# Kernel optimization log

Hardware: AMD Instinct MI355X
Metric: run time of the kernel (lower is better)

The kernel has to match this reference:

```python
import jax, jax.numpy as jnp
import numpy as np

# Algorithm constants (scaled-down but structure-identical to the source:
# original Nxy=2304, Nz=300, ItN=60, ROISize=300, NxyExt=128, BkgMean=110, SNR=200)
ItN = 2
BkgMean = 110.0
ROISize = 256
SNR = 200.0
NxyExt = 64
Nxy = 1024
Nz = 24
LO = Nxy // 2 - ROISize   # ROI start inside the padded FFT plane
HI = Nxy // 2 + ROISize   # ROI end


def setup_inputs() -> dict:
    key = jax.random.key(0)
    k1, k2, k3, k4 = jax.random.split(key, 4)
    # raw camera image; uniform in [0, 400) so that subtracting BkgMean=110 keeps signal
    imstack = jax.random.uniform(k1, (1, 1, Nxy - 2 * NxyExt, Nxy - 2 * NxyExt), dtype=jnp.float32) * 400.0
    # initial object volume estimate (the `init` ctor arg)
    init_vol = jax.random.uniform(k2, (1, Nz, 2 * ROISize, 2 * ROISize), dtype=jnp.float32)
    # learned frequency-domain PSF kernel (rand * 0.001, as in __init__)
    conv_real = jax.random.uniform(k3, (1, 1, Nxy, Nxy), dtype=jnp.float32) * 0.001
    conv_imag = jax.random.uniform(k4, (1, 1, Nxy, Nxy), dtype=jnp.float32) * 0.001
    return {"imstack": imstack, "init_vol": init_vol, "conv_real": conv_real, "conv_imag": conv_imag}


def reference(imstack, init_vol, conv_real, conv_imag):
    # Complex frequency-domain kernel; constant across iterations (the source
    # rebuilds/casts it every slice -- same math, hoisted here).
    K = (conv_real + 1j * conv_imag)[0, 0]            # [Nxy, Nxy] complex
    Ksum = jnp.sum(conv_real)

    img = jnp.maximum(imstack - BkgMean, 0.0)
    ImgExp = jnp.pad(img, ((0, 0), (0, 0), (NxyExt, NxyExt), (NxyExt, NxyExt)))  # [1,1,Nxy,Nxy]

    obj = init_vol                                     # [1, Nz, 2R, 2R]
    for _ in range(ItN):
        # --- forward projection: batched over all Nz slices (source loops) ---
        # each slice is placed into the center ROI of a zero [Nxy,Nxy] plane
        vol = jnp.pad(obj, ((0, 0), (0, 0), (LO, Nxy - HI), (LO, Nxy - HI)))  # [1,Nz,Nxy,Nxy]
        est = jnp.real(jnp.fft.ifft2(jnp.fft.fft2(vol) * K)) / Ksum
        ImgEst = jnp.sum(jnp.maximum(est, 0.0), axis=1, keepdims=True)        # [1,1,Nxy,Nxy]

        # --- ratio image (interior only; border stays 1) ---
        Tmp = jnp.median(ImgEst)
        inner = ImgExp[:, :, NxyExt:-NxyExt, NxyExt:-NxyExt] / (
            ImgEst[:, :, NxyExt:-NxyExt, NxyExt:-NxyExt] + Tmp / SNR)
        Ratio = jnp.ones((1, 1, Nxy, Nxy), dtype=ImgEst.dtype)
        Ratio = Ratio.at[:, :, NxyExt:-NxyExt, NxyExt:-NxyExt].set(inner)

        # --- back projection: in the source, fft2(Ratio)*conj(K) is identical for
        # every jj (Ratio and K do not change inside the loop), so compute once ---
        back = jnp.real(jnp.fft.ifft2(jnp.fft.fft2(Ratio) * jnp.conj(K))) / Ksum
        back = jnp.maximum(back, 0.0)                  # [1,1,Nxy,Nxy]
        obj = obj * back[:, :, LO:HI, LO:HI]           # broadcast over Nz
    return obj
```

## Files before the change

kernel.cpp:

```cpp
#include <hip/hip_runtime.h>
#include <math.h>

#define NXY  1024
#define NZ   24
#define ROI2 512
#define LO_  256
#define EXT  64
#define IMGW 896
#define ITN  2
#define SNR_ 200.0f
#define BKG  110.0f
#define RANK1 524287u
#define RANK2 524288u
#define NACC 8
#define PAD(i) ((i) + ((i) >> 4))

typedef float2 cf;

__device__ __forceinline__ cf cadd(cf a, cf b) { return make_float2(a.x + b.x, a.y + b.y); }
__device__ __forceinline__ cf csub(cf a, cf b) { return make_float2(a.x - b.x, a.y - b.y); }
__device__ __forceinline__ cf cmul(cf a, cf b) { return make_float2(a.x * b.x - a.y * b.y, a.x * b.y + a.y * b.x); }

__device__ __forceinline__ void twinit(cf* TW) {
  int k = threadIdx.x;
  float s, c;
  sincosf(-6.28318530717958647692f * (float)k / 1024.0f, &s, &c);
  TW[k] = make_float2(c, s);
}

template <int SIGN>
__device__ cf* fft1024_r4(cf* src, cf* dst, const cf* TW) {
  const int tid = threadIdx.x;
#pragma unroll
  for (int t = 0; t < 5; ++t) {
    __syncthreads();
    const int s = 1 << (2 * t);
    const int q = tid & (s - 1);
    const int sp = tid - q;
    cf a0 = src[PAD(tid)];
    cf a1 = src[PAD(tid + 256)];
    cf a2 = src[PAD(tid + 512)];
    cf a3 = src[PAD(tid + 768)];
    cf b0 = cadd(a0, a2), b1 = csub(a0, a2);
    cf b2 = cadd(a1, a3), b3 = csub(a1, a3);
    cf jb3 = (SIGN < 0) ? make_float2(b3.y, -b3.x) : make_float2(-b3.y, b3.x);
    cf c0 = cadd(b0, b2);
    cf c2 = csub(b0, b2);
    cf c1 = cadd(b1, jb3);
    cf c3 = csub(b1, jb3);
    cf t1v = TW[sp];
    if (SIGN > 0) t1v.y = -t1v.y;
    cf t2v = cmul(t1v, t1v);
    cf t3v = cmul(t2v, t1v);
    const int base = 4 * tid - 3 * q;
    dst[PAD(base)]         = c0;
    dst[PAD(base + s)]     = cmul(c1, t1v);
    dst[PAD(base + 2 * s)] = cmul(c2, t2v);
    dst[PAD(base + 3 * s)] = cmul(c3, t3v);
    cf* tmp = src; src = dst; dst = tmp;
  }
  __syncthreads();
  return src;
}

__global__ void ksum_kernel(const float* __restrict__ a, float* __restrict__ out) {
  __shared__ float s[256];
  int tid = threadIdx.x;
  float acc = 0.f;
  for (int i = blockIdx.x * 256 + tid; i < NXY * NXY; i += gridDim.x * 256) acc += a[i];
  s[tid] = acc;
  __syncthreads();
  for (int o = 128; o > 0; o >>= 1) {
    if (tid < o) s[tid] += s[tid + o];
    __syncthreads();
  }
  if (tid == 0) atomicAdd(out, s[0]);
}

__global__ void imgexp_kernel(const float* __restrict__ im, float* __restrict__ out) {
  int idx = blockIdx.x * 256 + threadIdx.x;
  int r = idx >> 10, c = idx & 1023;
  float v = 0.f;
  if (r >= EXT && r < NXY - EXT && c >= EXT && c < NXY - EXT) {
    float t = im[(size_t)(r - EXT) * IMGW + (c - EXT)] - BKG;
    v = t > 0.f ? t : 0.f;
  }
  out[idx] = v;
}

__global__ void buildkh_kernel(const float* __restrict__ kre, const float* __restrict__ kim,
                               cf* __restrict__ kt) {
  int idx = blockIdx.x * 256 + threadIdx.x;
  if (idx >= 513 * 1024) return;
  int ky = idx & 1023, kx = idx >> 10;
  int ny = (1024 - ky) & 1023, nx = (1024 - kx) & 1023;
  float ar = kre[(size_t)ky * NXY + kx], ai = kim[(size_t)ky * NXY + kx];
  float br = kre[(size_t)ny * NXY + nx], bi = kim[(size_t)ny * NXY + nx];
  kt[idx] = make_float2(0.5f * (ar + br), 0.5f * (ai - bi));
}

__global__ void transpose_kernel(const cf* __restrict__ in, cf* __restrict__ out, int R, int C) {
  __shared__ cf tile[32][33];
  size_t zoff = (size_t)blockIdx.z * R * C;
  const cf* src = in + zoff;
  cf* dst = out + zoff;
  int bc = blockIdx.x * 32, br = blockIdx.y * 32;
  int tx = threadIdx.x, ty = threadIdx.y;
#pragma unroll
  for (int j = 0; j < 32; j += 8) tile[ty + j][tx] = src[(size_t)(br + ty + j) * C + bc + tx];
  __syncthreads();
#pragma unroll
  for (int j = 0; j < 32; j += 8) dst[(size_t)(bc + ty + j) * R + br + tx] = tile[tx][ty + j];
}

__global__ __launch_bounds__(256) void pass1_kernel(const float* __restrict__ in, int rowLen, int rowOff,
                                                    cf* __restrict__ out) {
  __shared__ cf X[1088], Y[1088], TW[256];
  int tid = threadIdx.x;
  int b = blockIdx.x, zl = blockIdx.y;
  int nrows = 2 * gridDim.x;
  twinit(TW);
  const float* r0 = in + ((size_t)zl * nrows + 2 * b) * rowLen;
  const float* r1 = r0 + rowLen;
  for (int k = tid; k < 1024; k += 256) {
    cf v = make_float2(0.f, 0.f);
    if (k >= rowOff && k < rowOff + rowLen) { v.x = r0[k - rowOff]; v.y = r1[k - rowOff]; }
    X[PAD(k)] = v;
  }
  cf* G = fft1024_r4<-1>(X, Y, TW);
  cf* o0 = out + ((size_t)zl * nrows + 2 * b) * 512;
  cf* o1 = o0 + 512;
  for (int k = tid; k < 512; k += 256) {
    if (k == 0) {
      cf g0 = G[PAD(0)], gn = G[PAD(512)];
      o0[0] = make_float2(g0.x, gn.x);
      o1[0] = make_float2(g0.y, gn.y);
    } else {
      cf c = G[PAD(k)], d = G[PAD(1024 - k)];
      o0[k] = make_float2(0.5f * (c.x + d.x), 0.5f * (c.y - d.y));
      o1[k] = make_float2(0.5f * (c.y + d.y), 0.5f * (d.x - c.x));
    }
  }
}

__global__ __launch_bounds__(256) void pass1b_kernel(const float* __restrict__ iexp,
                                                     const float* __restrict__ iest,
                                                     const float* __restrict__ tos,
                                                     cf* __restrict__ out) {
  __shared__ cf X[1088], Y[1088], TW[256];
  int tid = threadIdx.x, b = blockIdx.x;
  twinit(TW);
  float t = tos[0];
  int r0 = 2 * b, r1 = 2 * b + 1;
  bool in0 = (r0 >= EXT && r0 < NXY - EXT);
  bool in1 = (r1 >= EXT && r1 < NXY - EXT);
  for (int k = tid; k < 1024; k += 256) {
    bool kin = (k >= EXT && k < NXY - EXT);
    float v0 = (in0 && kin) ? iexp[(size_t)r0 * NXY + k] / (iest[(size_t)r0 * NXY + k] + t) : 1.0f;
    float v1 = (in1 && kin) ? iexp[(size_t)r1 * NXY + k] / (iest[(size_t)r1 * NXY + k] + t) : 1.0f;
    X[PAD(k)] = make_float2(v0, v1);
  }
  cf* G = fft1024_r4<-1>(X, Y, TW);
  cf* o0 = out + (size_t)r0 * 512;
  cf* o1 = out + (size_t)r1 * 512;
  for (int k = tid; k < 512; k += 256) {
    if (k == 0) {
      cf g0 = G[PAD(0)], gn = G[PAD(512)];
      o0[0] = make_float2(g0.x, gn.x);
      o1[0] = make_float2(g0.y, gn.y);
    } else {
      cf c = G[PAD(k)], d = G[PAD(1024 - k)];
      o0[k] = make_float2(0.5f * (c.x + d.x), 0.5f * (c.y - d.y));
      o1[k] = make_float2(0.5f * (c.y + d.y), 0.5f * (d.x - c.x));
    }
  }
}

__global__ __launch_bounds__(256) void pass2_kernel(const cf* __restrict__ in, int inLen, int inOff,
                                                    const cf* __restrict__ kt, cf* __restrict__ out,
                                                    int zn, int ZB, int conjK) {
  __shared__ cf X[1088], Y[1088], TW[256];
  int tid = threadIdx.x;
  int kc = blockIdx.x;
  twinit(TW);
  const cf* krow = kt + (size_t)kc * NXY;
  cf kv[4];
#pragma unroll
  for (int j = 0; j < 4; ++j) {
    kv[j] = krow[tid + 256 * j];
    if (conjK) kv[j].y = -kv[j].y;
  }
  int srccol = (kc == 512) ? 0 : kc;
  int zlo = blockIdx.y * ZB, zhi = min(zn, zlo + ZB);
  for (int z = zlo; z < zhi; ++z) {
    const cf* src = in + ((size_t)z * 512 + srccol) * inLen;
    if (kc == 0 || kc == 512) {
      for (int k = tid; k < 1024; k += 256) {
        float v = 0.f;
        if (k >= inOff && k < inOff + inLen) {
          cf s = src[k - inOff];
          v = (kc == 0) ? s.x : s.y;
        }
        X[PAD(k)] = make_float2(v, 0.f);
      }
    } else {
      for (int k = tid; k < 1024; k += 256) {
        cf v = make_float2(0.f, 0.f);
        if (k >= inOff && k < inOff + inLen) v = src[k - inOff];
        X[PAD(k)] = v;
      }
    }
    cf* F = fft1024_r4<-1>(X, Y, TW);
#pragma unroll
    for (int j = 0; j < 4; ++j) {
      int p = PAD(tid + 256 * j);
      F[p] = cmul(F[p], kv[j]);
    }
    cf* G = fft1024_r4<1>(F, X, TW);
    cf* dstz = out + (size_t)z * 512 * NXY;
    if (kc == 0) {
      for (int k = tid; k < 1024; k += 256) dstz[k].x = G[PAD(k)].x;
    } else if (kc == 512) {
      for (int k = tid; k < 1024; k += 256) dstz[k].y = G[PAD(k)].x;
    } else {
      for (int k = tid; k < 1024; k += 256) dstz[(size_t)kc * NXY + k] = G[PAD(k)];
    }
    __syncthreads();
  }
}

__global__ __launch_bounds__(256) void pass3_fwd_kernel(const cf* __restrict__ in,
                                                        float* __restrict__ partials,
                                                        const float* __restrict__ ksump, int zn) {
  __shared__ cf X[1088], Y[1088], TW[256];
  int tid = threadIdx.x;
  int b = blockIdx.x, a = blockIdx.y;
  twinit(TW);
  float scale = 1.0f / (1048576.0f * ksump[0]);
  int r0 = 2 * b, r1 = 2 * b + 1;
  float acc[8] = {0.f, 0.f, 0.f, 0.f, 0.f, 0.f, 0.f, 0.f};
  for (int z = a; z < zn; z += NACC) {
    const cf* s0 = in + ((size_t)z * NXY + r0) * 512;
    const cf* s1 = s0 + 512;
    for (int k = tid; k < 512; k += 256) {
      cf u0 = s0[k], u1 = s1[k];
      if (k == 0) {
        X[PAD(0)]   = make_float2(u0.x, u1.x);
        X[PAD(512)] = make_float2(u0.y, u1.y);
      } else {
        X[PAD(k)]        = make_float2(u0.x - u1.y, u0.y + u1.x);
        X[PAD(1024 - k)] = make_float2(u0.x + u1.y, u1.x - u0.y);
      }
    }
    cf* G = fft1024_r4<1>(X, Y, TW);
#pragma unroll
    for (int j = 0; j < 4; ++j) {
      cf g = G[PAD(tid + 256 * j)];
      float v0 = g.x * scale, v1 = g.y * scale;
      acc[j]     += v0 > 0.f ? v0 : 0.f;
      acc[4 + j] += v1 > 0.f ? v1 : 0.f;
    }
    __syncthreads();
  }
  float* d0 = partials + ((size_t)a * NXY + r0) * NXY;
  float* d1 = d0 + NXY;
#pragma unroll
  for (int j = 0; j < 4; ++j) {
    d0[tid + 256 * j] += acc[j];
    d1[tid + 256 * j] += acc[4 + j];
  }
}

__global__ void fold_kernel(const float* __restrict__ partials, float* __restrict__ iest) {
  int i = blockIdx.x * 256 + threadIdx.x;
  float s = 0.f;
#pragma unroll
  for (int a = 0; a < NACC; ++a) s += partials[(size_t)a * NXY * NXY + i];
  iest[i] = s;
}

__global__ __launch_bounds__(256) void pass3_back_kernel(const cf* __restrict__ in, float* __restrict__ obj,
                                                         const float* __restrict__ ksump) {
  __shared__ cf X[1088], Y[1088], TW[256];
  __shared__ float br0[512], br1[512];
  int tid = threadIdx.x, b = blockIdx.x;
  twinit(TW);
  float scale = 1.0f / (1048576.0f * ksump[0]);
  int r0 = LO_ + 2 * b, r1 = r0 + 1;
  const cf* s0 = in + (size_t)r0 * 512;
  const cf* s1 = in + (size_t)r1 * 512;
  for (int k = tid; k < 512; k += 256) {
    cf u0 = s0[k], u1 = s1[k];
    if (k == 0) {
      X[PAD(0)]   = make_float2(u0.x, u1.x);
      X[PAD(512)] = make_float2(u0.y, u1.y);
    } else {
      X[PAD(k)]        = make_float2(u0.x - u1.y, u0.y + u1.x);
      X[PAD(1024 - k)] = make_float2(u0.x + u1.y, u1.x - u0.y);
    }
  }
  cf* G = fft1024_r4<1>(X, Y, TW);
  for (int k = tid; k < 512; k += 256) {
    cf g = G[PAD(k + LO_)];
    float v0 = g.x * scale, v1 = g.y * scale;
    br0[k] = v0 > 0.f ? v0 : 0.f;
    br1[k] = v1 > 0.f ? v1 : 0.f;
  }
  __syncthreads();
  int rp0 = 2 * b, rp1 = 2 * b + 1;
  for (int idx = tid; idx < NZ * 512; idx += 256) {
    int z = idx >> 9, c = idx & 511;
    obj[((size_t)z * ROI2 + rp0) * ROI2 + c] *= br0[c];
    obj[((size_t)z * ROI2 + rp1) * ROI2 + c] *= br1[c];
  }
}

__global__ void medinit_kernel(unsigned* st) {
  if (threadIdx.x == 0) { st[0] = 0u; st[1] = 0u; st[2] = RANK1; st[3] = RANK2; }
}

__global__ void medhist_kernel(const float* __restrict__ v, const unsigned* __restrict__ st,
                               unsigned* __restrict__ hist, int shift, unsigned maskHigh, int nb) {
  extern __shared__ unsigned h[];
  int tid = threadIdx.x;
  for (int k = tid; k < 2 * nb; k += 256) h[k] = 0u;
  __syncthreads();
  unsigned p1 = st[0], p2 = st[1];
  unsigned bm = (unsigned)(nb - 1);
  for (int i = blockIdx.x * 256 + tid; i < NXY * NXY; i += gridDim.x * 256) {
    unsigned u = __float_as_uint(v[i]);
    unsigned b = (u >> shift) & bm;
    if ((u & maskHigh) == (p1 & maskHigh)) atomicAdd(&h[b], 1u);
    if ((u & maskHigh) == (p2 & maskHigh)) atomicAdd(&h[nb + b], 1u);
  }
  __syncthreads();
  for (int k = tid; k < 2 * nb; k += 256) atomicAdd(&hist[k], h[k]);
}

__global__ void medpick_kernel(unsigned* st, const unsigned* __restrict__ hist, int shift, int nb,
                               int finalRound, float* tos) {
  __shared__ unsigned ps[256];
  int t = threadIdx.x;
  int per = nb >> 8;
  for (int which = 0; which < 2; ++which) {
    unsigned loc[8];
    unsigned my = 0;
    for (int i = 0; i < per; ++i) { loc[i] = hist[which * nb + t * per + i]; my += loc[i]; }
    ps[t] = my;
    __syncthreads();
    for (int off = 1; off < 256; off <<= 1) {
      unsigned v = (t >= off) ? ps[t - off] : 0u;
      __syncthreads();
      ps[t] += v;
      __syncthreads();
    }
    unsigned pre = ps[t] - my;
    unsigned r = st[2 + which];
    if (r >= pre && r < pre + my) {
      unsigned cum = pre;
      for (int i = 0; i < per; ++i) {
        if (r < cum + loc[i]) {
          st[which] |= (unsigned)(t * per + i) << shift;
          st[2 + which] = r - cum;
          break;
        }
        cum += loc[i];
      }
    }
    __syncthreads();
  }
  if (finalRound && t == 0) {
    float m = 0.5f * (__uint_as_float(st[0]) + __uint_as_float(st[1]));
    tos[0] = m / SNR_;
  }
}

extern "C" void kernel_launch(void* const* d_in, const int* in_sizes, int n_in,
                              void* d_out, int out_size, void* d_ws, size_t ws_size,
                              hipStream_t stream) {
  const float* imstack  = (const float*)d_in[0];
  const float* init_vol = (const float*)d_in[1];
  const float* conv_re  = (const float*)d_in[2];
  const float* conv_im  = (const float*)d_in[3];
  float* obj = (float*)d_out;

  char* w = (char*)d_ws;
  size_t off = 0;
  auto alloc = [&](size_t bytes) -> void* {
    void* p = (void*)(w + off);
    off += (bytes + 255) & ~(size_t)255;
    return p;
  };

  const size_t PLANE = (size_t)NXY * NXY;
  const size_t HPLANE = (size_t)512 * NXY;
  cf* KT         = (cf*)alloc((size_t)513 * NXY * sizeof(cf));
  float* IExp    = (float*)alloc(PLANE * 4);
  float* IEst    = (float*)alloc(PLANE * 4);
  float* Partial = (float*)alloc((size_t)NACC * PLANE * 4);
  float* Ksum    = (float*)alloc(256);
  unsigned* St   = (unsigned*)alloc(256);
  unsigned* Hist = (unsigned*)alloc(2 * 2048 * 4);
  size_t fixedEnd = off;

  int ZC = 1;
  const int zcs[8] = {24, 12, 8, 6, 4, 3, 2, 1};
  for (int i = 0; i < 8; ++i) {
    size_t need = fixedEnd + (size_t)zcs[i] * 2ull * HPLANE * sizeof(cf) + 4096;
    if (need <= ws_size) { ZC = zcs[i]; break; }
  }
  cf* bufC = (cf*)alloc((size_t)ZC * HPLANE * sizeof(cf));
  cf* bufD = (cf*)alloc((size_t)ZC * HPLANE * sizeof(cf));
  float* Tos = Ksum + 1;

  hipMemcpyAsync(obj, init_vol, (size_t)NZ * ROI2 * ROI2 * 4, hipMemcpyDeviceToDevice, stream);
  hipMemsetAsync(Ksum, 0, 8, stream);
  ksum_kernel<<<256, 256, 0, stream>>>(conv_re, Ksum);
  imgexp_kernel<<<4096, 256, 0, stream>>>(imstack, IExp);
  buildkh_kernel<<<2052, 256, 0, stream>>>(conv_re, conv_im, KT);

  const int shifts[3] = {21, 10, 0};
  const int nbs[3]    = {2048, 2048, 1024};
  const unsigned masks[3] = {0u, 0xFFE00000u, 0xFFFFFC00u};

  for (int it = 0; it < ITN; ++it) {
    hipMemsetAsync(Partial, 0, (size_t)NACC * PLANE * 4, stream);
    for (int z0 = 0; z0 < NZ; z0 += ZC) {
      int zn = (NZ - z0 < ZC) ? (NZ - z0) : ZC;
      int nzb = (zn + 3) / 4;
      pass1_kernel<<<dim3(256, zn), 256, 0, stream>>>(obj + (size_t)z0 * ROI2 * ROI2, ROI2, LO_, bufC);
      transpose_kernel<<<dim3(16, 16, zn), dim3(32, 8), 0, stream>>>(bufC, bufD, 512, 512);
      pass2_kernel<<<dim3(513, nzb), 256, 0, stream>>>(bufD, 512, LO_, KT, bufC, zn, 4, 0);
      transpose_kernel<<<dim3(32, 16, zn), dim3(32, 8), 0, stream>>>(bufC, bufD, 512, 1024);
      pass3_fwd_kernel<<<dim3(512, NACC), 256, 0, stream>>>(bufD, Partial, Ksum, zn);
    }
    fold_kernel<<<4096, 256, 0, stream>>>(Partial, IEst);
    medinit_kernel<<<1, 64, 0, stream>>>(St);
    for (int round = 0; round < 3; ++round) {
      hipMemsetAsync(Hist, 0, 2 * 2048 * 4, stream);
      medhist_kernel<<<256, 256, 2 * nbs[round] * 4, stream>>>(IEst, St, Hist, shifts[round],
                                                               masks[round], nbs[round]);
      medpick_kernel<<<1, 256, 0, stream>>>(St, Hist, shifts[round], nbs[round],
                                            round == 2 ? 1 : 0, Tos);
    }
    pass1b_kernel<<<512, 256, 0, stream>>>(IExp, IEst, Tos, bufC);
    transpose_kernel<<<dim3(16, 32, 1), dim3(32, 8), 0, stream>>>(bufC, bufD, 1024, 512);
    pass2_kernel<<<dim3(513, 1), 256, 0, stream>>>(bufD, 1024, 0, KT, bufC, 1, 1, 1);
    transpose_kernel<<<dim3(32, 16, 1), dim3(32, 8), 0, stream>>>(bufC, bufD, 512, 1024);
    pass3_back_kernel<<<256, 256, 0, stream>>>(bufD, obj, Ksum);
  }
}
```

Before: 705.9 us.

## Prune zero-input FFT stages, merge Nyquist columns, swizzle LDS, trim launches

```diff
diff --git a/kernel.cpp b/kernel.cpp
--- a/kernel.cpp
+++ b/kernel.cpp
@@ -12,8 +12,8 @@
 #define BKG  110.0f
 #define RANK1 524287u
 #define RANK2 524288u
-#define NACC 8
-#define PAD(i) ((i) + ((i) >> 4))
+#define NACC 4
+#define SWZ(i) ((i) ^ ((((i) >> 4) & 3) * 5))
 
 typedef float2 cf;
 
@@ -21,26 +21,31 @@
 __device__ __forceinline__ cf csub(cf a, cf b) { return make_float2(a.x - b.x, a.y - b.y); }
 __device__ __forceinline__ cf cmul(cf a, cf b) { return make_float2(a.x * b.x - a.y * b.y, a.x * b.y + a.y * b.x); }
 
-__device__ __forceinline__ void twinit(cf* TW) {
+struct Tw { const cf *t0, *t1, *t2, *t3; };
+
+__device__ __forceinline__ void twinit_all(cf* TW0, cf* T1, cf* T2, cf* T3) {
+  const float W = -6.28318530717958647692f / 1024.0f;
   int k = threadIdx.x;
   float s, c;
-  sincosf(-6.28318530717958647692f * (float)k / 1024.0f, &s, &c);
-  TW[k] = make_float2(c, s);
-}
-
-template <int SIGN>
-__device__ cf* fft1024_r4(cf* src, cf* dst, const cf* TW) {
+  sincosf(W * (float)k, &s, &c);
+  TW0[k] = make_float2(c, s);
+  if (k < 64) { sincosf(W * (float)(4 * k), &s, &c);  T1[k] = make_float2(c, s); }
+  if (k < 16) { sincosf(W * (float)(16 * k), &s, &c); T2[k] = make_float2(c, s); }
+  if (k < 4)  { sincosf(W * (float)(64 * k), &s, &c); T3[k] = make_float2(c, s); }
+}
+
+template <int SIGN, int T0>
+__device__ cf* fft1024_r4_t(cf* src, cf* dst, Tw tw) {
   const int tid = threadIdx.x;
 #pragma unroll
-  for (int t = 0; t < 5; ++t) {
+  for (int t = T0; t < 5; ++t) {
     __syncthreads();
     const int s = 1 << (2 * t);
     const int q = tid & (s - 1);
-    const int sp = tid - q;
-    cf a0 = src[PAD(tid)];
-    cf a1 = src[PAD(tid + 256)];
-    cf a2 = src[PAD(tid + 512)];
-    cf a3 = src[PAD(tid + 768)];
+    cf a0 = src[SWZ(tid)];
+    cf a1 = src[SWZ(tid + 256)];
+    cf a2 = src[SWZ(tid + 512)];
+    cf a3 = src[SWZ(tid + 768)];
     cf b0 = cadd(a0, a2), b1 = csub(a0, a2);
     cf b2 = cadd(a1, a3), b3 = csub(a1, a3);
     cf jb3 = (SIGN < 0) ? make_float2(b3.y, -b3.x) : make_float2(-b3.y, b3.x);
@@ -48,19 +53,45 @@
     cf c2 = csub(b0, b2);
     cf c1 = cadd(b1, jb3);
     cf c3 = csub(b1, jb3);
-    cf t1v = TW[sp];
-    if (SIGN > 0) t1v.y = -t1v.y;
-    cf t2v = cmul(t1v, t1v);
-    cf t3v = cmul(t2v, t1v);
     const int base = 4 * tid - 3 * q;
-    dst[PAD(base)]         = c0;
-    dst[PAD(base + s)]     = cmul(c1, t1v);
-    dst[PAD(base + 2 * s)] = cmul(c2, t2v);
-    dst[PAD(base + 3 * s)] = cmul(c3, t3v);
+    if (t == 4) {
+      dst[SWZ(base)]         = c0;
+      dst[SWZ(base + s)]     = c1;
+      dst[SWZ(base + 2 * s)] = c2;
+      dst[SWZ(base + 3 * s)] = c3;
+    } else {
+      cf t1v = (t == 0) ? tw.t0[tid] : (t == 1) ? tw.t1[tid >> 2]
+             : (t == 2) ? tw.t2[tid >> 4] : tw.t3[tid >> 6];
+      if (SIGN > 0) t1v.y = -t1v.y;
+      cf t2v = cmul(t1v, t1v);
+      cf t3v = cmul(t2v, t1v);
+      dst[SWZ(base)]         = c0;
+      dst[SWZ(base + s)]     = cmul(c1, t1v);
+      dst[SWZ(base + 2 * s)] = cmul(c2, t2v);
+      dst[SWZ(base + 3 * s)] = cmul(c3, t3v);
+    }
     cf* tmp = src; src = dst; dst = tmp;
   }
   __syncthreads();
   return src;
+}
+
+__device__ __forceinline__ void fft_stage0_half(cf a1, cf a2, cf* dst, const cf* TW0) {
+  const int tid = threadIdx.x;
+  cf b1 = make_float2(-a2.x, -a2.y);
+  cf jb3 = make_float2(a1.y, -a1.x);
+  cf c0 = cadd(a2, a1);
+  cf c2 = csub(a2, a1);
+  cf c1 = cadd(b1, jb3);
+  cf c3 = csub(b1, jb3);
+  cf t1v = TW0[tid];
+  cf t2v = cmul(t1v, t1v);
+  cf t3v = cmul(t2v, t1v);
+  const int base = 4 * tid;
+  dst[SWZ(base)]     = c0;
+  dst[SWZ(base + 1)] = cmul(c1, t1v);
+  dst[SWZ(base + 2)] = cmul(c2, t2v);
+  dst[SWZ(base + 3)] = cmul(c3, t3v);
 }
 
 __global__ void ksum_kernel(const float* __restrict__ a, float* __restrict__ out) {
@@ -113,30 +144,26 @@
   for (int j = 0; j < 32; j += 8) dst[(size_t)(bc + ty + j) * R + br + tx] = tile[tx][ty + j];
 }
 
-__global__ __launch_bounds__(256) void pass1_kernel(const float* __restrict__ in, int rowLen, int rowOff,
-                                                    cf* __restrict__ out) {
-  __shared__ cf X[1088], Y[1088], TW[256];
-  int tid = threadIdx.x;
-  int b = blockIdx.x, zl = blockIdx.y;
-  int nrows = 2 * gridDim.x;
-  twinit(TW);
-  const float* r0 = in + ((size_t)zl * nrows + 2 * b) * rowLen;
-  const float* r1 = r0 + rowLen;
-  for (int k = tid; k < 1024; k += 256) {
-    cf v = make_float2(0.f, 0.f);
-    if (k >= rowOff && k < rowOff + rowLen) { v.x = r0[k - rowOff]; v.y = r1[k - rowOff]; }
-    X[PAD(k)] = v;
-  }
-  cf* G = fft1024_r4<-1>(X, Y, TW);
-  cf* o0 = out + ((size_t)zl * nrows + 2 * b) * 512;
+__global__ __launch_bounds__(256) void pass1_kernel(const float* __restrict__ in, cf* __restrict__ out) {
+  __shared__ cf X[1024], Y[1024], TW0[256], T1[64], T2[16], T3[4];
+  int tid = threadIdx.x, b = blockIdx.x, zl = blockIdx.y;
+  twinit_all(TW0, T1, T2, T3);
+  const float* r0 = in + ((size_t)zl * 512 + 2 * b) * 512;
+  const float* r1 = r0 + 512;
+  cf a1 = make_float2(r0[tid], r1[tid]);
+  cf a2 = make_float2(r0[tid + 256], r1[tid + 256]);
+  fft_stage0_half(a1, a2, Y, TW0);
+  Tw tw{TW0, T1, T2, T3};
+  cf* G = fft1024_r4_t<-1, 1>(Y, X, tw);
+  cf* o0 = out + ((size_t)zl * 512 + 2 * b) * 512;
   cf* o1 = o0 + 512;
   for (int k = tid; k < 512; k += 256) {
     if (k == 0) {
-      cf g0 = G[PAD(0)], gn = G[PAD(512)];
+      cf g0 = G[SWZ(0)], gn = G[SWZ(512)];
       o0[0] = make_float2(g0.x, gn.x);
       o1[0] = make_float2(g0.y, gn.y);
     } else {
-      cf c = G[PAD(k)], d = G[PAD(1024 - k)];
+      cf c = G[SWZ(k)], d = G[SWZ(1024 - k)];
       o0[k] = make_float2(0.5f * (c.x + d.x), 0.5f * (c.y - d.y));
       o1[k] = make_float2(0.5f * (c.y + d.y), 0.5f * (d.x - c.x));
     }
@@ -147,9 +174,9 @@
                                                      const float* __restrict__ iest,
                                                      const float* __restrict__ tos,
                                                      cf* __restrict__ out) {
-  __shared__ cf X[1088], Y[1088], TW[256];
+  __shared__ cf X[1024], Y[1024], TW0[256], T1[64], T2[16], T3[4];
   int tid = threadIdx.x, b = blockIdx.x;
-  twinit(TW);
+  twinit_all(TW0, T1, T2, T3);
   float t = tos[0];
   int r0 = 2 * b, r1 = 2 * b + 1;
   bool in0 = (r0 >= EXT && r0 < NXY - EXT);
@@ -158,84 +185,98 @@
     bool kin = (k >= EXT && k < NXY - EXT);
     float v0 = (in0 && kin) ? iexp[(size_t)r0 * NXY + k] / (iest[(size_t)r0 * NXY + k] + t) : 1.0f;
     float v1 = (in1 && kin) ? iexp[(size_t)r1 * NXY + k] / (iest[(size_t)r1 * NXY + k] + t) : 1.0f;
-    X[PAD(k)] = make_float2(v0, v1);
-  }
-  cf* G = fft1024_r4<-1>(X, Y, TW);
+    X[SWZ(k)] = make_float2(v0, v1);
+  }
+  Tw tw{TW0, T1, T2, T3};
+  cf* G = fft1024_r4_t<-1, 0>(X, Y, tw);
   cf* o0 = out + (size_t)r0 * 512;
   cf* o1 = out + (size_t)r1 * 512;
   for (int k = tid; k < 512; k += 256) {
     if (k == 0) {
-      cf g0 = G[PAD(0)], gn = G[PAD(512)];
+      cf g0 = G[SWZ(0)], gn = G[SWZ(512)];
       o0[0] = make_float2(g0.x, gn.x);
       o1[0] = make_float2(g0.y, gn.y);
     } else {
-      cf c = G[PAD(k)], d = G[PAD(1024 - k)];
+      cf c = G[SWZ(k)], d = G[SWZ(1024 - k)];
       o0[k] = make_float2(0.5f * (c.x + d.x), 0.5f * (c.y - d.y));
       o1[k] = make_float2(0.5f * (c.y + d.y), 0.5f * (d.x - c.x));
     }
   }
 }
 
-__global__ __launch_bounds__(256) void pass2_kernel(const cf* __restrict__ in, int inLen, int inOff,
+template <int HALFIN>
+__global__ __launch_bounds__(256) void pass2_kernel(const cf* __restrict__ in,
                                                     const cf* __restrict__ kt, cf* __restrict__ out,
                                                     int zn, int ZB, int conjK) {
-  __shared__ cf X[1088], Y[1088], TW[256];
-  int tid = threadIdx.x;
-  int kc = blockIdx.x;
-  twinit(TW);
-  const cf* krow = kt + (size_t)kc * NXY;
-  cf kv[4];
+  __shared__ cf X[1024], Y[1024], TW0[256], T1[64], T2[16], T3[4];
+  int tid = threadIdx.x, kc = blockIdx.x;
+  twinit_all(TW0, T1, T2, T3);
+  Tw tw{TW0, T1, T2, T3};
+  cf kva[4], kvb[4];
 #pragma unroll
   for (int j = 0; j < 4; ++j) {
-    kv[j] = krow[tid + 256 * j];
-    if (conjK) kv[j].y = -kv[j].y;
-  }
-  int srccol = (kc == 512) ? 0 : kc;
+    kva[j] = kt[(size_t)kc * NXY + tid + 256 * j];
+    if (conjK) kva[j].y = -kva[j].y;
+  }
+  if (kc == 0) {
+#pragma unroll
+    for (int j = 0; j < 4; ++j) {
+      kvb[j] = kt[(size_t)512 * NXY + tid + 256 * j];
+      if (conjK) kvb[j].y = -kvb[j].y;
+    }
+  }
+  const int inLen = HALFIN ? 512 : 1024;
   int zlo = blockIdx.y * ZB, zhi = min(zn, zlo + ZB);
   for (int z = zlo; z < zhi; ++z) {
-    const cf* src = in + ((size_t)z * 512 + srccol) * inLen;
-    if (kc == 0 || kc == 512) {
-      for (int k = tid; k < 1024; k += 256) {
-        float v = 0.f;
-        if (k >= inOff && k < inOff + inLen) {
-          cf s = src[k - inOff];
-          v = (kc == 0) ? s.x : s.y;
-        }
-        X[PAD(k)] = make_float2(v, 0.f);
+    const cf* src = in + ((size_t)z * 512 + kc) * inLen;
+    cf* F;
+    if (HALFIN) {
+      cf a1 = src[tid], a2 = src[tid + 256];
+      fft_stage0_half(a1, a2, Y, TW0);
+      F = fft1024_r4_t<-1, 1>(Y, X, tw);
+    } else {
+      for (int k = tid; k < 1024; k += 256) X[SWZ(k)] = src[k];
+      F = fft1024_r4_t<-1, 0>(X, Y, tw);
+    }
+    if (kc == 0) {
+      cf fk[4], fn[4];
+#pragma unroll
+      for (int j = 0; j < 4; ++j) {
+        int k = tid + 256 * j, nk = (1024 - k) & 1023;
+        fk[j] = F[SWZ(k)];
+        fn[j] = F[SWZ(nk)];
       }
-    } else {
-      for (int k = tid; k < 1024; k += 256) {
-        cf v = make_float2(0.f, 0.f);
-        if (k >= inOff && k < inOff + inLen) v = src[k - inOff];
-        X[PAD(k)] = v;
+      __syncthreads();
+#pragma unroll
+      for (int j = 0; j < 4; ++j) {
+        int k = tid + 256 * j;
+        cf Fa = make_float2(0.5f * (fk[j].x + fn[j].x), 0.5f * (fk[j].y - fn[j].y));
+        cf Fb = make_float2(0.5f * (fk[j].y + fn[j].y), 0.5f * (fn[j].x - fk[j].x));
+        cf Ga = cmul(Fa, kva[j]);
+        cf Gb = cmul(Fb, kvb[j]);
+        F[SWZ(k)] = make_float2(Ga.x - Gb.y, Ga.y + Gb.x);
       }
-    }
-    cf* F = fft1024_r4<-1>(X, Y, TW);
-#pragma unroll
-    for (int j = 0; j < 4; ++j) {
-      int p = PAD(tid + 256 * j);
-      F[p] = cmul(F[p], kv[j]);
-    }
-    cf* G = fft1024_r4<1>(F, X, TW);
-    cf* dstz = out + (size_t)z * 512 * NXY;
-    if (kc == 0) {
-      for (int k = tid; k < 1024; k += 256) dstz[k].x = G[PAD(k)].x;
-    } else if (kc == 512) {
-      for (int k = tid; k < 1024; k += 256) dstz[k].y = G[PAD(k)].x;
-    } else {
-      for (int k = tid; k < 1024; k += 256) dstz[(size_t)kc * NXY + k] = G[PAD(k)];
-    }
-    __syncthreads();
+    } else {
+#pragma unroll
+      for (int j = 0; j < 4; ++j) {
+        int p = SWZ(tid + 256 * j);
+        F[p] = cmul(F[p], kva[j]);
+      }
+    }
+    cf* G = fft1024_r4_t<1, 0>(F, (F == X) ? Y : X, tw);
+    cf* dst = out + ((size_t)z * 512 + kc) * NXY;
+    for (int k = tid; k < 1024; k += 256) dst[k] = G[SWZ(k)];
   }
 }
 
 __global__ __launch_bounds__(256) void pass3_fwd_kernel(const cf* __restrict__ in,
                                                         float* __restrict__ partials,
-                                                        const float* __restrict__ ksump, int zn) {
-  __shared__ cf X[1088], Y[1088], TW[256];
-  int tid = threadIdx.x;
-  int b = blockIdx.x, a = blockIdx.y;
-  twinit(TW);
+                                                        const float* __restrict__ ksump, int zn,
+                                                        int accum) {
+  __shared__ cf X[1024], Y[1024], TW0[256], T1[64], T2[16], T3[4];
+  int tid = threadIdx.x, b = blockIdx.x, a = blockIdx.y;
+  twinit_all(TW0, T1, T2, T3);
+  Tw tw{TW0, T1, T2, T3};
   float scale = 1.0f / (1048576.0f * ksump[0]);
   int r0 = 2 * b, r1 = 2 * b + 1;
   float acc[8] = {0.f, 0.f, 0.f, 0.f, 0.f, 0.f, 0.f, 0.f};
@@ -245,46 +286,50 @@
     for (int k = tid; k < 512; k += 256) {
       cf u0 = s0[k], u1 = s1[k];
       if (k == 0) {
-        X[PAD(0)]   = make_float2(u0.x, u1.x);
-        X[PAD(512)] = make_float2(u0.y, u1.y);
+        X[SWZ(0)]   = make_float2(u0.x, u1.x);
+        X[SWZ(512)] = make_float2(u0.y, u1.y);
       } else {
-        X[PAD(k)]        = make_float2(u0.x - u1.y, u0.y + u1.x);
-        X[PAD(1024 - k)] = make_float2(u0.x + u1.y, u1.x - u0.y);
+        X[SWZ(k)]        = make_float2(u0.x - u1.y, u0.y + u1.x);
+        X[SWZ(1024 - k)] = make_float2(u0.x + u1.y, u1.x - u0.y);
       }
     }
-    cf* G = fft1024_r4<1>(X, Y, TW);
+    cf* G = fft1024_r4_t<1, 0>(X, Y, tw);
 #pragma unroll
     for (int j = 0; j < 4; ++j) {
-      cf g = G[PAD(tid + 256 * j)];
+      cf g = G[SWZ(tid + 256 * j)];
       float v0 = g.x * scale, v1 = g.y * scale;
       acc[j]     += v0 > 0.f ? v0 : 0.f;
       acc[4 + j] += v1 > 0.f ? v1 : 0.f;
     }
-    __syncthreads();
   }
   float* d0 = partials + ((size_t)a * NXY + r0) * NXY;
   float* d1 = d0 + NXY;
-#pragma unroll
-  for (int j = 0; j < 4; ++j) {
-    d0[tid + 256 * j] += acc[j];
-    d1[tid + 256 * j] += acc[4 + j];
-  }
-}
-
-__global__ void fold_kernel(const float* __restrict__ partials, float* __restrict__ iest) {
+  if (accum) {
+#pragma unroll
+    for (int j = 0; j < 4; ++j) { d0[tid + 256 * j] += acc[j]; d1[tid + 256 * j] += acc[4 + j]; }
+  } else {
+#pragma unroll
+    for (int j = 0; j < 4; ++j) { d0[tid + 256 * j] = acc[j]; d1[tid + 256 * j] = acc[4 + j]; }
+  }
+}
+
+__global__ void fold_kernel(const float* __restrict__ partials, float* __restrict__ iest,
+                            unsigned* __restrict__ st) {
   int i = blockIdx.x * 256 + threadIdx.x;
   float s = 0.f;
 #pragma unroll
   for (int a = 0; a < NACC; ++a) s += partials[(size_t)a * NXY * NXY + i];
   iest[i] = s;
+  if (i == 0) { st[0] = 0u; st[1] = 0u; st[2] = RANK1; st[3] = RANK2; }
 }
 
 __global__ __launch_bounds__(256) void pass3_back_kernel(const cf* __restrict__ in, float* __restrict__ obj,
                                                          const float* __restrict__ ksump) {
-  __shared__ cf X[1088], Y[1088], TW[256];
+  __shared__ cf X[1024], Y[1024], TW0[256], T1[64], T2[16], T3[4];
   __shared__ float br0[512], br1[512];
   int tid = threadIdx.x, b = blockIdx.x;
-  twinit(TW);
+  twinit_all(TW0, T1, T2, T3);
+  Tw tw{TW0, T1, T2, T3};
   float scale = 1.0f / (1048576.0f * ksump[0]);
   int r0 = LO_ + 2 * b, r1 = r0 + 1;
   const cf* s0 = in + (size_t)r0 * 512;
@@ -292,16 +337,16 @@
   for (int k = tid; k < 512; k += 256) {
     cf u0 = s0[k], u1 = s1[k];
     if (k == 0) {
-      X[PAD(0)]   = make_float2(u0.x, u1.x);
-      X[PAD(512)] = make_float2(u0.y, u1.y);
-    } else {
-      X[PAD(k)]        = make_float2(u0.x - u1.y, u0.y + u1.x);
-      X[PAD(1024 - k)] = make_float2(u0.x + u1.y, u1.x - u0.y);
-    }
-  }
-  cf* G = fft1024_r4<1>(X, Y, TW);
+      X[SWZ(0)]   = make_float2(u0.x, u1.x);
+      X[SWZ(512)] = make_float2(u0.y, u1.y);
+    } else {
+      X[SWZ(k)]        = make_float2(u0.x - u1.y, u0.y + u1.x);
+      X[SWZ(1024 - k)] = make_float2(u0.x + u1.y, u1.x - u0.y);
+    }
+  }
+  cf* G = fft1024_r4_t<1, 0>(X, Y, tw);
   for (int k = tid; k < 512; k += 256) {
-    cf g = G[PAD(k + LO_)];
+    cf g = G[SWZ(k + LO_)];
     float v0 = g.x * scale, v1 = g.y * scale;
     br0[k] = v0 > 0.f ? v0 : 0.f;
     br1[k] = v1 > 0.f ? v1 : 0.f;
@@ -313,10 +358,6 @@
     obj[((size_t)z * ROI2 + rp0) * ROI2 + c] *= br0[c];
     obj[((size_t)z * ROI2 + rp1) * ROI2 + c] *= br1[c];
   }
-}
-
-__global__ void medinit_kernel(unsigned* st) {
-  if (threadIdx.x == 0) { st[0] = 0u; st[1] = 0u; st[2] = RANK1; st[3] = RANK2; }
 }
 
 __global__ void medhist_kernel(const float* __restrict__ v, const unsigned* __restrict__ st,
@@ -400,12 +441,12 @@
   float* Partial = (float*)alloc((size_t)NACC * PLANE * 4);
   float* Ksum    = (float*)alloc(256);
   unsigned* St   = (unsigned*)alloc(256);
-  unsigned* Hist = (unsigned*)alloc(2 * 2048 * 4);
+  unsigned* Hist = (unsigned*)alloc(3 * 2 * 2048 * 4);
   size_t fixedEnd = off;
 
-  int ZC = 1;
-  const int zcs[8] = {24, 12, 8, 6, 4, 3, 2, 1};
-  for (int i = 0; i < 8; ++i) {
+  int ZC = 2;
+  const int zcs[7] = {24, 12, 8, 6, 4, 3, 2};
+  for (int i = 0; i < 7; ++i) {
     size_t need = fixedEnd + (size_t)zcs[i] * 2ull * HPLANE * sizeof(cf) + 4096;
     if (need <= ws_size) { ZC = zcs[i]; break; }
   }
@@ -424,28 +465,26 @@
   const unsigned masks[3] = {0u, 0xFFE00000u, 0xFFFFFC00u};
 
   for (int it = 0; it < ITN; ++it) {
-    hipMemsetAsync(Partial, 0, (size_t)NACC * PLANE * 4, stream);
     for (int z0 = 0; z0 < NZ; z0 += ZC) {
       int zn = (NZ - z0 < ZC) ? (NZ - z0) : ZC;
-      int nzb = (zn + 3) / 4;
-      pass1_kernel<<<dim3(256, zn), 256, 0, stream>>>(obj + (size_t)z0 * ROI2 * ROI2, ROI2, LO_, bufC);
+      int nzb = (zn + 5) / 6;
+      pass1_kernel<<<dim3(256, zn), 256, 0, stream>>>(obj + (size_t)z0 * ROI2 * ROI2, bufC);
       transpose_kernel<<<dim3(16, 16, zn), dim3(32, 8), 0, stream>>>(bufC, bufD, 512, 512);
-      pass2_kernel<<<dim3(513, nzb), 256, 0, stream>>>(bufD, 512, LO_, KT, bufC, zn, 4, 0);
+      pass2_kernel<1><<<dim3(512, nzb), 256, 0, stream>>>(bufD, KT, bufC, zn, 6, 0);
       transpose_kernel<<<dim3(32, 16, zn), dim3(32, 8), 0, stream>>>(bufC, bufD, 512, 1024);
-      pass3_fwd_kernel<<<dim3(512, NACC), 256, 0, stream>>>(bufD, Partial, Ksum, zn);
-    }
-    fold_kernel<<<4096, 256, 0, stream>>>(Partial, IEst);
-    medinit_kernel<<<1, 64, 0, stream>>>(St);
+      pass3_fwd_kernel<<<dim3(512, NACC), 256, 0, stream>>>(bufD, Partial, Ksum, zn, z0 > 0 ? 1 : 0);
+    }
+    fold_kernel<<<4096, 256, 0, stream>>>(Partial, IEst, St);
+    hipMemsetAsync(Hist, 0, 3 * 2 * 2048 * 4, stream);
     for (int round = 0; round < 3; ++round) {
-      hipMemsetAsync(Hist, 0, 2 * 2048 * 4, stream);
-      medhist_kernel<<<256, 256, 2 * nbs[round] * 4, stream>>>(IEst, St, Hist, shifts[round],
-                                                               masks[round], nbs[round]);
-      medpick_kernel<<<1, 256, 0, stream>>>(St, Hist, shifts[round], nbs[round],
+      medhist_kernel<<<256, 256, 2 * nbs[round] * 4, stream>>>(IEst, St, Hist + round * 4096,
+                                                               shifts[round], masks[round], nbs[round]);
+      medpick_kernel<<<1, 256, 0, stream>>>(St, Hist + round * 4096, shifts[round], nbs[round],
                                             round == 2 ? 1 : 0, Tos);
     }
     pass1b_kernel<<<512, 256, 0, stream>>>(IExp, IEst, Tos, bufC);
     transpose_kernel<<<dim3(16, 32, 1), dim3(32, 8), 0, stream>>>(bufC, bufD, 1024, 512);
-    pass2_kernel<<<dim3(513, 1), 256, 0, stream>>>(bufD, 1024, 0, KT, bufC, 1, 1, 1);
+    pass2_kernel<0><<<dim3(512, 1), 256, 0, stream>>>(bufD, KT, bufC, 1, 1, 1);
     transpose_kernel<<<dim3(32, 16, 1), dim3(32, 8), 0, stream>>>(bufC, bufD, 512, 1024);
     pass3_back_kernel<<<256, 256, 0, stream>>>(bufD, obj, Ksum);
   }
```

After: 632.8 us. -10.4%, faster.
